# Kernel optimization log

Hardware: AMD Instinct MI355X
Metric: run time of the kernel (lower is better)

The kernel has to match this reference:

```python
import jax, jax.numpy as jnp
import numpy as np
import math

EPS = float(jnp.finfo(jnp.float32).eps)


def _mask_imag(z, n_ops):
    # Zero the imaginary part of (b,c) slices whose relative imaginary
    # magnitude is below the FFT roundoff threshold (vectorized version of
    # the original per-(i,j) Python loop).
    re, im = z.real, z.imag
    max_im = jnp.max(jnp.abs(im), axis=(-2, -1), keepdims=True)
    max_abs = jnp.max(jnp.abs(z), axis=(-2, -1), keepdims=True)
    mask = (max_im / max_abs) <= (n_ops * EPS)
    im = jnp.where(mask, jnp.zeros_like(im), im)
    return jax.lax.complex(re, im)


def otf2psf(otf, outsize):
    h, w = otf.shape[-2], otf.shape[-1]
    n_ops = h * w * (math.log2(h) + math.log2(w))
    psf = jnp.fft.ifft2(otf)
    psf = _mask_imag(psf, n_ops)
    psf = jnp.roll(psf, (outsize[0] // 2, outsize[1] // 2), axis=(-2, -1))
    return psf[..., : outsize[0], : outsize[1]]


def psf2otf(psf, shape):
    p0, p1 = psf.shape[-2], psf.shape[-1]
    n_ops = p0 * p1 * (math.log2(p0) + math.log2(p1))
    pad = [(0, 0)] * (psf.ndim - 2) + [(0, shape[0] - p0), (0, shape[1] - p1)]
    otf = jnp.pad(psf, pad)
    otf = jnp.roll(otf, (-(p0 // 2), -(p1 // 2)), axis=(-2, -1))
    otf = jnp.fft.fft2(otf)
    return _mask_imag(otf, n_ops)


def compute_ax(psf, latent_ft, image_size, psf_size_2d, gamma):
    xf = psf2otf(psf, image_size)          # [b, cp, H, W] complex
    y = jnp.real(otf2psf(latent_ft * xf, psf_size_2d))  # [b, c, p, p]
    return y + gamma * psf


def conjgrad(x, latent_ft, b_rhs, n_iter, image_size, psf_size_2d, gamma):
    r = b_rhs - compute_ax(x, latent_ft, image_size, psf_size_2d, gamma)
    p = r
    rsold = jnp.sum(r * r, axis=(-2, -1), keepdims=True)
    for _ in range(n_iter):  # small fixed iteration count
        Ap = compute_ax(p, latent_ft, image_size, psf_size_2d, gamma)
        alpha = rsold / jnp.sum(p * Ap, axis=(-2, -1), keepdims=True)
        x = x + alpha * p
        r = r - alpha * Ap
        rsnew = jnp.sum(r * r, axis=(-2, -1), keepdims=True)
        p = r + (rsnew / rsold) * p
        rsold = rsnew
    return x


def setup_inputs() -> dict:
    key = jax.random.key(0)
    k1, k2, k3, k4 = jax.random.split(key, 4)
    shape = (4, 3, 512, 512)
    return {
        "blurx": jax.random.normal(k1, shape, dtype=jnp.float32),
        "blury": jax.random.normal(k2, shape, dtype=jnp.float32),
        "latentx": jax.random.normal(k3, shape, dtype=jnp.float32),
        "latenty": jax.random.normal(k4, shape, dtype=jnp.float32),
        "psf_size": 31,
    }


def reference(blurx, blury, latentx, latenty, psf_size):
    n_iter = 10
    gamma = 1.0
    blur = jnp.sqrt(blurx ** 2 + blury ** 2)
    latent = jnp.sqrt(latentx ** 2 + latenty ** 2)
    b, c, h, w = blur.shape
    kernel = jnp.full((b, 1, psf_size, psf_size), 1.0 / float(psf_size ** 2), dtype=blur.dtype)
    blur_f = jnp.fft.fft2(blur)
    latent_f = jnp.fft.fft2(latent)
    bf = jnp.conj(latent_f) * blur_f
    latent_ft = jnp.conj(latent_f) * latent_f
    blur_otf = jnp.real(otf2psf(bf, (psf_size, psf_size)))  # [b, c, p, p]
    kernel = conjgrad(kernel, latent_ft, blur_otf, n_iter, (h, w), (psf_size, psf_size), gamma)
    # threshold small entries, clamp negatives, normalize
    kf = kernel.reshape(b, c, -1)
    max_var = jnp.max(kf, axis=2, keepdims=True)
    kf = jnp.where(kf < 0.05 * max_var, jnp.zeros_like(kf), kf)
    kernel = kf.reshape(b, c, psf_size, psf_size)
    kernel = jnp.where(kernel < 0, jnp.zeros_like(kernel), kernel)
    kernel = kernel / jnp.sum(kernel, axis=(-2, -1), keepdims=True)
    return kernel
```

## Files before the change

### kernel.cpp

```cpp
#include <hip/hip_runtime.h>
#include <math.h>

#define NIMG 12
#define NN 512
#define NPIX (NN * NN)

__device__ __forceinline__ int brev9(int p) {
  return (int)(__brev((unsigned)p) >> 23);
}

__device__ __forceinline__ void fft512_core(
    float vr[8], float vi[8], const int inv,
    const float* __restrict__ twr, const float* __restrict__ twi,
    const int lane)
{
#pragma unroll
  for (int s = 0; s < 3; ++s) {
    const int half = 1 << s;
#pragma unroll
    for (int e = 0; e < 8; ++e) {
      if ((e & half) == 0) {
        const int j = (e & (half - 1)) << (8 - s);
        const float wr = twr[j];
        const float wi = inv ? -twi[j] : twi[j];
        const float br = vr[e + half], bi = vi[e + half];
        const float tr = __fsub_rn(__fmul_rn(wr, br), __fmul_rn(wi, bi));
        const float ti = __fadd_rn(__fmul_rn(wr, bi), __fmul_rn(wi, br));
        vr[e + half] = __fsub_rn(vr[e], tr); vi[e + half] = __fsub_rn(vi[e], ti);
        vr[e] = __fadd_rn(vr[e], tr); vi[e] = __fadd_rn(vi[e], ti);
      }
    }
  }
#pragma unroll
  for (int s = 3; s <= 8; ++s) {
    const int xm = 1 << (s - 3);
    const bool low = (lane & xm) == 0;
#pragma unroll
    for (int e = 0; e < 8; ++e) {
      const float orr = __shfl_xor(vr[e], xm);
      const float oii = __shfl_xor(vi[e], xm);
      const int j = ((((lane & (xm - 1)) << 3) | e)) << (8 - s);
      const float wr = twr[j];
      const float wi = inv ? -twi[j] : twi[j];
      if (low) {
        const float tr = __fsub_rn(__fmul_rn(wr, orr), __fmul_rn(wi, oii));
        const float ti = __fadd_rn(__fmul_rn(wr, oii), __fmul_rn(wi, orr));
        vr[e] = __fadd_rn(vr[e], tr); vi[e] = __fadd_rn(vi[e], ti);
      } else {
        const float tr = __fsub_rn(__fmul_rn(wr, vr[e]), __fmul_rn(wi, vi[e]));
        const float ti = __fadd_rn(__fmul_rn(wr, vi[e]), __fmul_rn(wi, vr[e]));
        vr[e] = __fsub_rn(orr, tr); vi[e] = __fsub_rn(oii, ti);
      }
    }
  }
  if (inv) {
    const float sc = 1.0f / 512.0f;
#pragma unroll
    for (int e = 0; e < 8; ++e) {
      vr[e] = __fmul_rn(vr[e], sc); vi[e] = __fmul_rn(vi[e], sc);
    }
  }
}

__device__ __forceinline__ float np_pw_base(const float* a, int n)
{
  float r0 = a[0], r1 = a[1], r2 = a[2], r3 = a[3];
  float r4 = a[4], r5 = a[5], r6 = a[6], r7 = a[7];
  int i = 8;
  const int lim = n - (n & 7);
  for (; i < lim; i += 8) {
    r0 = __fadd_rn(r0, a[i + 0]); r1 = __fadd_rn(r1, a[i + 1]);
    r2 = __fadd_rn(r2, a[i + 2]); r3 = __fadd_rn(r3, a[i + 3]);
    r4 = __fadd_rn(r4, a[i + 4]); r5 = __fadd_rn(r5, a[i + 5]);
    r6 = __fadd_rn(r6, a[i + 6]); r7 = __fadd_rn(r7, a[i + 7]);
  }
  float res = __fadd_rn(
      __fadd_rn(__fadd_rn(r0, r1), __fadd_rn(r2, r3)),
      __fadd_rn(__fadd_rn(r4, r5), __fadd_rn(r6, r7)));
  for (; i < n; ++i) res = __fadd_rn(res, a[i]);
  return res;
}

__global__ __launch_bounds__(256) void twiddle_kernel(float2* __restrict__ twg)
{
  const int k = threadIdx.x;
  double s, c;
  sincos(-2.0 * M_PI * (double)k / 512.0, &s, &c);
  twg[k] = make_float2((float)c, (float)s);
}

__global__ __launch_bounds__(256) void loadmag_kernel(
    const float* __restrict__ bx, const float* __restrict__ by,
    const float* __restrict__ lx, const float* __restrict__ ly,
    float2* __restrict__ B2, float2* __restrict__ B1)
{
  const int i = blockIdx.x * 256 + threadIdx.x;
  {
    const float a = lx[i], b = ly[i];
    const float s = __fadd_rn(__fmul_rn(a, a), __fmul_rn(b, b));
    B2[i] = make_float2((float)sqrt((double)s), 0.f);
  }
  {
    const float a = bx[i], b = by[i];
    const float s = __fadd_rn(__fmul_rn(a, a), __fmul_rn(b, b));
    B1[i] = make_float2((float)sqrt((double)s), 0.f);
  }
}

__global__ __launch_bounds__(256) void rowfft_kernel(
    float2* __restrict__ A, float2* __restrict__ B,
    const float2* __restrict__ twg)
{
  __shared__ float twr[256], twi[256];
  { const float2 t = twg[threadIdx.x]; twr[threadIdx.x] = t.x; twi[threadIdx.x] = t.y; }
  __syncthreads();
  int wid = blockIdx.x * 4 + (threadIdx.x >> 6);
  const int lane = threadIdx.x & 63;
  float2* buf = A;
  if (wid >= NIMG * NN) { wid -= NIMG * NN; buf = B; }
  const int base = (wid >> 9) * NPIX + (wid & 511) * NN;
  float vr[8], vi[8];
#pragma unroll
  for (int e = 0; e < 8; ++e) {
    const float2 z = buf[base + brev9(lane * 8 + e)];
    vr[e] = z.x; vi[e] = z.y;
  }
  fft512_core(vr, vi, 0, twr, twi, lane);
#pragma unroll
  for (int e = 0; e < 8; ++e)
    buf[base + lane * 8 + e] = make_float2(vr[e], vi[e]);
}

__global__ __launch_bounds__(256) void colA_kernel(
    float2* __restrict__ B2, const float2* __restrict__ twg)
{
  __shared__ float twr[256], twi[256];
  __shared__ float2 ld[4][520];
  { const float2 t = twg[threadIdx.x]; twr[threadIdx.x] = t.x; twi[threadIdx.x] = t.y; }
  const int img = blockIdx.x >> 7;
  const int c0  = (blockIdx.x & 127) * 4;
  const int tid = threadIdx.x;
  float2* __restrict__ base = B2 + img * NPIX;
  for (int it = 0; it < 8; ++it) {
    const int idx = it * 256 + tid;
    ld[idx & 3][idx >> 2] = base[(idx >> 2) * NN + c0 + (idx & 3)];
  }
  __syncthreads();
  const int w = tid >> 6, lane = tid & 63;
  float vr[8], vi[8];
#pragma unroll
  for (int e = 0; e < 8; ++e) {
    const float2 z = ld[w][brev9(lane * 8 + e)];
    vr[e] = z.x; vi[e] = z.y;
  }
  fft512_core(vr, vi, 0, twr, twi, lane);
#pragma unroll
  for (int e = 0; e < 8; ++e) ld[w][lane * 8 + e] = make_float2(vr[e], vi[e]);
  __syncthreads();
  for (int it = 0; it < 8; ++it) {
    const int idx = it * 256 + tid;
    base[(idx >> 2) * NN + c0 + (idx & 3)] = ld[idx & 3][idx >> 2];
  }
}

__global__ __launch_bounds__(256) void colB_kernel(
    const float2* __restrict__ B1, float2* __restrict__ B3,
    const float2* __restrict__ twg)
{
  __shared__ float twr[256], twi[256];
  __shared__ float2 ld[4][520];
  { const float2 t = twg[threadIdx.x]; twr[threadIdx.x] = t.x; twi[threadIdx.x] = t.y; }
  const int img = blockIdx.x >> 7;
  const int c0  = (blockIdx.x & 127) * 4;
  const int tid = threadIdx.x;
  const float2* __restrict__ in = B1 + img * NPIX;
  for (int it = 0; it < 8; ++it) {
    const int idx = it * 256 + tid;
    ld[idx & 3][idx >> 2] = in[(idx >> 2) * NN + c0 + (idx & 3)];
  }
  __syncthreads();
  const int w = tid >> 6, lane = tid & 63;
  const int c = c0 + w;
  float vr[8], vi[8];
#pragma unroll
  for (int e = 0; e < 8; ++e) {
    const float2 z = ld[w][brev9(lane * 8 + e)];
    vr[e] = z.x; vi[e] = z.y;
  }
  fft512_core(vr, vi, 0, twr, twi, lane);
  float2* __restrict__ out = B3 + img * NPIX + c * NN + lane * 8;
#pragma unroll
  for (int e = 0; e < 8; ++e) out[e] = make_float2(vr[e], vi[e]);
}

__global__ __launch_bounds__(256) void fp_kernel(
    const float2* __restrict__ B2, float* __restrict__ FP)
{
  const int i = blockIdx.x * 256 + threadIdx.x;
  const float2 l = B2[i];
  FP[i] = __fadd_rn(__fmul_rn(l.x, l.x), __fmul_rn(l.y, l.y));
}

__global__ __launch_bounds__(256) void kb_kernel(
    const float2* __restrict__ R, float2* __restrict__ B3,
    unsigned* __restrict__ stats, const float2* __restrict__ twg)
{
  __shared__ float twr[256], twi[256];
  __shared__ float smi[4], sma[4];
  { const float2 t = twg[threadIdx.x]; twr[threadIdx.x] = t.x; twi[threadIdx.x] = t.y; }
  __syncthreads();
  const int img = blockIdx.x >> 7;
  const int c   = (blockIdx.x & 127) * 4 + (threadIdx.x >> 6);
  const int lane = threadIdx.x & 63;
  float vr[8], vi[8];
#pragma unroll
  for (int e = 0; e < 8; ++e) {
    const int q = brev9(lane * 8 + e);
    const int k = (q + 15) & 511;
    if (k < 31) {
      const float2 z = R[(img * 31 + k) * NN + c];
      vr[e] = z.x; vi[e] = z.y;
    } else { vr[e] = 0.f; vi[e] = 0.f; }
  }
  fft512_core(vr, vi, 0, twr, twi, lane);
  float mi = 0.f, ma = 0.f;
#pragma unroll
  for (int e = 0; e < 8; ++e) {
    mi = fmaxf(mi, fabsf(vi[e]));
    const float ab = (float)sqrt(
        (double)__fadd_rn(__fmul_rn(vr[e], vr[e]), __fmul_rn(vi[e], vi[e])));
    ma = fmaxf(ma, ab);
  }
#pragma unroll
  for (int off = 32; off; off >>= 1) {
    mi = fmaxf(mi, __shfl_xor(mi, off));
    ma = fmaxf(ma, __shfl_xor(ma, off));
  }
  if (lane == 0) { smi[threadIdx.x >> 6] = mi; sma[threadIdx.x >> 6] = ma; }
  float2* __restrict__ out = B3 + img * NPIX + c * NN + lane * 8;
#pragma unroll
  for (int e = 0; e < 8; ++e) out[e] = make_float2(vr[e], vi[e]);
  __syncthreads();
  if (threadIdx.x == 0) {
    mi = fmaxf(fmaxf(smi[0], smi[1]), fmaxf(smi[2], smi[3]));
    ma = fmaxf(fmaxf(sma[0], sma[1]), fmaxf(sma[2], sma[3]));
    atomicMax(&stats[img * 2 + 0], __float_as_uint(mi));
    atomicMax(&stats[img * 2 + 1], __float_as_uint(ma));
  }
}

__global__ __launch_bounds__(256) void kprod_kernel(
    const float2* __restrict__ B3, const float2* __restrict__ B2,
    const float* __restrict__ FP, float2* __restrict__ Y,
    const unsigned* __restrict__ stats, const float2* __restrict__ twg,
    int bmode)
{
  __shared__ float twr[256], twi[256];
  __shared__ float2 ldx[8][520];
  { const float2 t = twg[threadIdx.x]; twr[threadIdx.x] = t.x; twi[threadIdx.x] = t.y; }
  const int img = blockIdx.x >> 6;
  const int r0  = (blockIdx.x & 63) * 8;
  const int tid = threadIdx.x;
  const float2* __restrict__ X = B3 + img * NPIX;
  for (int it = 0; it < 16; ++it) {
    const int idx = it * 256 + tid;
    ldx[idx & 7][idx >> 3] = X[(idx >> 3) * NN + r0 + (idx & 7)];
  }
  bool fire = false;
  if (bmode == 0) {
    const float m1 = __uint_as_float(stats[img * 2 + 0]);
    const float m2 = __uint_as_float(stats[img * 2 + 1]);
    const double MTHR =
        961.0 * (log2(31.0) + log2(31.0)) * 1.1920928955078125e-7;
    fire = ((double)__fdiv_rn(m1, m2) <= MTHR);
  }
  __syncthreads();
  const int w = tid >> 6, lane = tid & 63;
  for (int rep = 0; rep < 2; ++rep) {
    const int r_l = w + 4 * rep;
    const int r = r0 + r_l;
    float vr[8], vi[8];
    if (bmode) {
      const float2* __restrict__ Lrow = B2 + img * NPIX + r * NN;
#pragma unroll
      for (int e = 0; e < 8; ++e) {
        const int q = brev9(lane * 8 + e);
        const float2 xb = ldx[r_l][q];
        const float2 l  = Lrow[q];
        vr[e] = __fadd_rn(__fmul_rn(l.x, xb.x), __fmul_rn(l.y, xb.y));
        vi[e] = __fsub_rn(__fmul_rn(l.x, xb.y), __fmul_rn(l.y, xb.x));
      }
    } else {
      const float* __restrict__ Frow = FP + img * NPIX + r * NN;
#pragma unroll
      for (int e = 0; e < 8; ++e) {
        const int q = brev9(lane * 8 + e);
        const float2 xb = ldx[r_l][q];
        const float fi = fire ? 0.f : xb.y;
        const float F  = Frow[q];
        vr[e] = __fmul_rn(F, xb.x);
        vi[e] = __fmul_rn(F, fi);
      }
    }
    fft512_core(vr, vi, 1, twr, twi, lane);
#pragma unroll
    for (int e = 0; e < 8; ++e) {
      const int c2 = lane * 8 + e;
      if (c2 >= 497 || c2 <= 15) {
        const int v = (c2 + 15) & 511;
        Y[(img * 31 + v) * NN + r] = make_float2(vr[e], vi[e]);
      }
    }
  }
}

__global__ __launch_bounds__(256) void kA_kernel(
    const float2* __restrict__ Y, float* __restrict__ yv,
    const float2* __restrict__ twg)
{
  __shared__ float twr[256], twi[256];
  { const float2 t = twg[threadIdx.x]; twr[threadIdx.x] = t.x; twi[threadIdx.x] = t.y; }
  __syncthreads();
  const int wid = blockIdx.x * 4 + (threadIdx.x >> 6);
  if (wid >= NIMG * 31) return;
  const int lane = threadIdx.x & 63;
  const int img = wid / 31, v = wid - img * 31;
  const float2* __restrict__ Yv = Y + (img * 31 + v) * NN;
  float vr[8], vi[8];
#pragma unroll
  for (int e = 0; e < 8; ++e) {
    const float2 z = Yv[brev9(lane * 8 + e)];
    vr[e] = z.x; vi[e] = z.y;
  }
  fft512_core(vr, vi, 1, twr, twi, lane);
#pragma unroll
  for (int e = 0; e < 8; ++e) {
    const int q2 = lane * 8 + e;
    const int u = (q2 + 15) & 511;
    if (u < 31) yv[img * 961 + u * 31 + v] = vr[e];
  }
}

__global__ __launch_bounds__(1024) void kC_kernel(
    const float* __restrict__ yv, float2* __restrict__ R,
    float* __restrict__ bvec, float* __restrict__ xv,
    float* __restrict__ rv, float* __restrict__ pv,
    float* __restrict__ rsoldg, unsigned* __restrict__ stats,
    const float2* __restrict__ twg, float* __restrict__ out,
    int mode, int fin)
{
  __shared__ float twr[256], twi[256];
  __shared__ float pl[961], prodl[961];
  __shared__ float pwl[8], redf[16];
  __shared__ float scal;
  const int tid = threadIdx.x;
  const int wave = tid >> 6, lane = tid & 63;
  const int img = blockIdx.x;
  if (tid < 256) { const float2 t = twg[tid]; twr[tid] = t.x; twi[tid] = t.y; }
  __syncthreads();

  const bool act = tid < 961;
  const int g = img * 961 + tid;

  auto pairwise = [&]() -> float {
    __syncthreads();
    if (tid < 8) pwl[tid] = np_pw_base(prodl + tid * 120, (tid == 7) ? 121 : 120);
    __syncthreads();
    if (tid == 0) {
      const float L = __fadd_rn(__fadd_rn(pwl[0], pwl[1]), __fadd_rn(pwl[2], pwl[3]));
      const float Rr = __fadd_rn(__fadd_rn(pwl[4], pwl[5]), __fadd_rn(pwl[6], pwl[7]));
      scal = __fadd_rn(L, Rr);
    }
    __syncthreads();
    const float s = scal;
    __syncthreads();
    return s;
  };

  if (mode == 2) {
    if (act) {
      bvec[g] = yv[g];
      xv[g] = (float)(1.0 / 961.0);
      pl[tid] = (float)(1.0 / 961.0);
    }
  } else if (mode == 0) {
    if (act) {
      const float Ap = __fadd_rn(yv[g], xv[g]);
      const float r0 = __fsub_rn(bvec[g], Ap);
      rv[g] = r0; pv[g] = r0; pl[tid] = r0;
      prodl[tid] = __fmul_rn(r0, r0);
    }
    const float s = pairwise();
    if (tid == 0) rsoldg[img] = s;
  } else {
    float p = 0.f, Ap = 0.f, nr = 0.f;
    if (act) {
      p = pv[g];
      Ap = __fadd_rn(yv[g], p);
      prodl[tid] = __fmul_rn(p, Ap);
    }
    const float pAp = pairwise();
    if (tid == 0) scal = rsoldg[img] / pAp;
    __syncthreads();
    const float alpha = scal;
    __syncthreads();
    if (act) {
      xv[g] = __fadd_rn(xv[g], __fmul_rn(alpha, p));
      nr = __fsub_rn(rv[g], __fmul_rn(alpha, Ap));
      rv[g] = nr;
      prodl[tid] = __fmul_rn(nr, nr);
    }
    const float rsnew = pairwise();
    if (tid == 0) { scal = rsnew / rsoldg[img]; rsoldg[img] = rsnew; }
    __syncthreads();
    const float beta = scal;
    __syncthreads();
    if (act) {
      const float pn = __fadd_rn(nr, __fmul_rn(beta, p));
      pv[g] = pn; pl[tid] = pn;
    }
  }
  if (tid == 0) { stats[img * 2 + 0] = 0u; stats[img * 2 + 1] = 0u; }
  __syncthreads();

  if (fin) {
    const float x = act ? xv[g] : -3.4e38f;
    float v = x;
#pragma unroll
    for (int off = 32; off; off >>= 1) v = fmaxf(v, __shfl_xor(v, off));
    if (lane == 0) redf[wave] = v;
    __syncthreads();
    if (tid == 0) {
      float s = redf[0];
      for (int w2 = 1; w2 < 16; ++w2) s = fmaxf(s, redf[w2]);
      scal = s;
    }
    __syncthreads();
    const float maxv = scal;
    const float thrf = __fmul_rn(0.05f, maxv);
    float vvv = act ? x : 0.f;
    if (vvv < thrf) vvv = 0.f;
    if (vvv < 0.f)  vvv = 0.f;
    if (act) prodl[tid] = vvv;
    const float ssum = pairwise();
    if (act) out[g] = vvv / ssum;
    return;
  }

  for (int rep = 0; rep < 2; ++rep) {
    const int k = wave + 16 * rep;
    if (k < 31) {
      float vr[8], vi[8];
#pragma unroll
      for (int e = 0; e < 8; ++e) {
        const int q = brev9(lane * 8 + e);
        const int l = (q + 15) & 511;
        vr[e] = (l < 31) ? pl[k * 31 + l] : 0.f;
        vi[e] = 0.f;
      }
      fft512_core(vr, vi, 0, twr, twi, lane);
      float2* __restrict__ Rk = R + (img * 31 + k) * NN + lane * 8;
#pragma unroll
      for (int e = 0; e < 8; ++e) Rk[e] = make_float2(vr[e], vi[e]);
    }
  }
}

extern "C" void kernel_launch(void* const* d_in, const int* in_sizes, int n_in,
                              void* d_out, int out_size, void* d_ws, size_t ws_size,
                              hipStream_t stream)
{
  const float* bx = (const float*)d_in[0];
  const float* by = (const float*)d_in[1];
  const float* lx = (const float*)d_in[2];
  const float* ly = (const float*)d_in[3];

  float* ws = (float*)d_ws;
  float2* B1 = (float2*)ws;
  float2* B2 = B1 + (size_t)NIMG * NPIX;
  float2* B3 = B2 + (size_t)NIMG * NPIX;
  float2* R  = B3 + (size_t)NIMG * NPIX;
  float2* Y  = R  + (size_t)NIMG * 31 * NN;
  float*  FP = (float*)(Y + (size_t)NIMG * 31 * NN);
  float*  vec = FP + (size_t)NIMG * NPIX;
  float*  bvec = vec;
  float*  xv   = bvec + NIMG * 961;
  float*  rv   = xv   + NIMG * 961;
  float*  pv   = rv   + NIMG * 961;
  float*  yv   = pv   + NIMG * 961;
  float*  rsold = yv  + NIMG * 961;
  unsigned* stats = (unsigned*)(rsold + NIMG);
  float2* twg = (float2*)(stats + 24);
  float* out = (float*)d_out;

  twiddle_kernel<<<1, 256, 0, stream>>>(twg);
  loadmag_kernel<<<NIMG * NPIX / 256, 256, 0, stream>>>(bx, by, lx, ly, B2, B1);
  rowfft_kernel<<<2 * NIMG * NN / 4, 256, 0, stream>>>(B2, B1, twg);
  colA_kernel<<<NIMG * 128, 256, 0, stream>>>(B2, twg);
  colB_kernel<<<NIMG * 128, 256, 0, stream>>>(B1, B3, twg);
  fp_kernel<<<NIMG * NPIX / 256, 256, 0, stream>>>(B2, FP);
  kprod_kernel<<<NIMG * 64, 256, 0, stream>>>(B3, B2, FP, Y, stats, twg, 1);
  kA_kernel<<<(NIMG * 31 + 3) / 4, 256, 0, stream>>>(Y, yv, twg);
  kC_kernel<<<NIMG, 1024, 0, stream>>>(yv, R, bvec, xv, rv, pv, rsold, stats,
                                       twg, out, 2, 0);

  for (int a = 0; a < 11; ++a) {
    kb_kernel<<<NIMG * 128, 256, 0, stream>>>(R, B3, stats, twg);
    kprod_kernel<<<NIMG * 64, 256, 0, stream>>>(B3, B2, FP, Y, stats, twg, 0);
    kA_kernel<<<(NIMG * 31 + 3) / 4, 256, 0, stream>>>(Y, yv, twg);
    const int mode = (a == 0) ? 0 : 1;
    const int fin  = (a == 10) ? 1 : 0;
    kC_kernel<<<NIMG, 1024, 0, stream>>>(yv, R, bvec, xv, rv, pv, rsold, stats,
                                         twg, out, mode, fin);
  }
}
```

Measured before the change: 1.458 ms.

## Exploit Hermitian symmetry to store and compute only half the column FFT spectrum

The column FFT kernels (colB, kb) now compute and store only columns 0..256 of the real-input spectrum, roughly halving their FFT work and memory writes. kprod rebuilds the other half on the fly from conjugate-symmetric entries, loading paired rows r and 512-r into a shared tile so each block handles 16 rows. This cuts global traffic and FFT work in the repeated CG loop. The cost is more complex indexing, a larger shared tile, fewer kprod blocks, and a dependence on the inputs to those FFTs being real.

```diff
diff --git a/kernel.cpp b/kernel.cpp
--- a/kernel.cpp
+++ b/kernel.cpp
@@ -4,6 +4,7 @@
 #define NIMG 12
 #define NN 512
 #define NPIX (NN * NN)
+#define XST (257 * 512)
 
 __device__ __forceinline__ int brev9(int p) {
   return (int)(__brev((unsigned)p) >> 23);
@@ -164,23 +165,25 @@
 }
 
 __global__ __launch_bounds__(256) void colB_kernel(
-    const float2* __restrict__ B1, float2* __restrict__ B3,
+    const float2* __restrict__ B1, float2* __restrict__ XH,
     const float2* __restrict__ twg)
 {
   __shared__ float twr[256], twi[256];
   __shared__ float2 ld[4][520];
   { const float2 t = twg[threadIdx.x]; twr[threadIdx.x] = t.x; twi[threadIdx.x] = t.y; }
-  const int img = blockIdx.x >> 7;
-  const int c0  = (blockIdx.x & 127) * 4;
+  const int img = blockIdx.x / 65;
+  const int c0  = (blockIdx.x % 65) * 4;
   const int tid = threadIdx.x;
   const float2* __restrict__ in = B1 + img * NPIX;
   for (int it = 0; it < 8; ++it) {
     const int idx = it * 256 + tid;
-    ld[idx & 3][idx >> 2] = in[(idx >> 2) * NN + c0 + (idx & 3)];
+    const int cc = c0 + (idx & 3);
+    ld[idx & 3][idx >> 2] = in[(idx >> 2) * NN + (cc < NN ? cc : NN - 1)];
   }
   __syncthreads();
   const int w = tid >> 6, lane = tid & 63;
   const int c = c0 + w;
+  if (c > 256) return;
   float vr[8], vi[8];
 #pragma unroll
   for (int e = 0; e < 8; ++e) {
@@ -188,7 +191,7 @@
     vr[e] = z.x; vi[e] = z.y;
   }
   fft512_core(vr, vi, 0, twr, twi, lane);
-  float2* __restrict__ out = B3 + img * NPIX + c * NN + lane * 8;
+  float2* __restrict__ out = XH + (size_t)img * XST + c * NN + lane * 8;
 #pragma unroll
   for (int e = 0; e < 8; ++e) out[e] = make_float2(vr[e], vi[e]);
 }
@@ -202,34 +205,39 @@
 }
 
 __global__ __launch_bounds__(256) void kb_kernel(
-    const float2* __restrict__ R, float2* __restrict__ B3,
+    const float2* __restrict__ R, float2* __restrict__ XH,
     unsigned* __restrict__ stats, const float2* __restrict__ twg)
 {
   __shared__ float twr[256], twi[256];
   __shared__ float smi[4], sma[4];
   { const float2 t = twg[threadIdx.x]; twr[threadIdx.x] = t.x; twi[threadIdx.x] = t.y; }
   __syncthreads();
-  const int img = blockIdx.x >> 7;
-  const int c   = (blockIdx.x & 127) * 4 + (threadIdx.x >> 6);
+  const int img = blockIdx.x / 65;
+  const int c   = (blockIdx.x % 65) * 4 + (threadIdx.x >> 6);
   const int lane = threadIdx.x & 63;
-  float vr[8], vi[8];
-#pragma unroll
-  for (int e = 0; e < 8; ++e) {
-    const int q = brev9(lane * 8 + e);
-    const int k = (q + 15) & 511;
-    if (k < 31) {
-      const float2 z = R[(img * 31 + k) * NN + c];
-      vr[e] = z.x; vi[e] = z.y;
-    } else { vr[e] = 0.f; vi[e] = 0.f; }
-  }
-  fft512_core(vr, vi, 0, twr, twi, lane);
   float mi = 0.f, ma = 0.f;
-#pragma unroll
-  for (int e = 0; e < 8; ++e) {
-    mi = fmaxf(mi, fabsf(vi[e]));
-    const float ab = (float)sqrt(
-        (double)__fadd_rn(__fmul_rn(vr[e], vr[e]), __fmul_rn(vi[e], vi[e])));
-    ma = fmaxf(ma, ab);
+  if (c <= 256) {
+    float vr[8], vi[8];
+#pragma unroll
+    for (int e = 0; e < 8; ++e) {
+      const int q = brev9(lane * 8 + e);
+      const int k = (q + 15) & 511;
+      if (k < 31) {
+        const float2 z = R[(img * 31 + k) * NN + c];
+        vr[e] = z.x; vi[e] = z.y;
+      } else { vr[e] = 0.f; vi[e] = 0.f; }
+    }
+    fft512_core(vr, vi, 0, twr, twi, lane);
+#pragma unroll
+    for (int e = 0; e < 8; ++e) {
+      mi = fmaxf(mi, fabsf(vi[e]));
+      const float ab = (float)sqrt(
+          (double)__fadd_rn(__fmul_rn(vr[e], vr[e]), __fmul_rn(vi[e], vi[e])));
+      ma = fmaxf(ma, ab);
+    }
+    float2* __restrict__ out = XH + (size_t)img * XST + c * NN + lane * 8;
+#pragma unroll
+    for (int e = 0; e < 8; ++e) out[e] = make_float2(vr[e], vi[e]);
   }
 #pragma unroll
   for (int off = 32; off; off >>= 1) {
@@ -237,9 +245,6 @@
     ma = fmaxf(ma, __shfl_xor(ma, off));
   }
   if (lane == 0) { smi[threadIdx.x >> 6] = mi; sma[threadIdx.x >> 6] = ma; }
-  float2* __restrict__ out = B3 + img * NPIX + c * NN + lane * 8;
-#pragma unroll
-  for (int e = 0; e < 8; ++e) out[e] = make_float2(vr[e], vi[e]);
   __syncthreads();
   if (threadIdx.x == 0) {
     mi = fmaxf(fmaxf(smi[0], smi[1]), fmaxf(smi[2], smi[3]));
@@ -250,21 +255,27 @@
 }
 
 __global__ __launch_bounds__(256) void kprod_kernel(
-    const float2* __restrict__ B3, const float2* __restrict__ B2,
+    const float2* __restrict__ XH, const float2* __restrict__ B2,
     const float* __restrict__ FP, float2* __restrict__ Y,
     const unsigned* __restrict__ stats, const float2* __restrict__ twg,
     int bmode)
 {
   __shared__ float twr[256], twi[256];
-  __shared__ float2 ldx[8][520];
+  __shared__ float2 T[17][257];
   { const float2 t = twg[threadIdx.x]; twr[threadIdx.x] = t.x; twi[threadIdx.x] = t.y; }
-  const int img = blockIdx.x >> 6;
-  const int r0  = (blockIdx.x & 63) * 8;
+  const int img = blockIdx.x >> 5;
+  const int g   = blockIdx.x & 31;
   const int tid = threadIdx.x;
-  const float2* __restrict__ X = B3 + img * NPIX;
-  for (int it = 0; it < 16; ++it) {
-    const int idx = it * 256 + tid;
-    ldx[idx & 7][idx >> 3] = X[(idx >> 3) * NN + r0 + (idx & 7)];
+  const float2* __restrict__ Xi = XH + (size_t)img * XST;
+  const int base1 = 8 * g;
+  const int base2 = (g == 0) ? 504 : (505 - 8 * g);
+  for (int idx = tid; idx < 257 * 16; idx += 256) {
+    const int c = idx >> 4, sub = idx & 15;
+    const int row = (sub < 8) ? (base1 + (sub & 7)) : (base2 + (sub & 7));
+    T[sub][c] = Xi[c * NN + row];
+  }
+  if (g == 0) {
+    for (int c = tid; c < 257; c += 256) T[16][c] = Xi[c * NN + 256];
   }
   bool fire = false;
   if (bmode == 0) {
@@ -276,17 +287,28 @@
   }
   __syncthreads();
   const int w = tid >> 6, lane = tid & 63;
-  for (int rep = 0; rep < 2; ++rep) {
-    const int r_l = w + 4 * rep;
-    const int r = r0 + r_l;
+  for (int t = 0; t < 4; ++t) {
+    const int oi = w + 4 * t;
+    int r, slot_r, slot_m;
+    if (g == 0) {
+      if (oi < 8)       { r = oi;       slot_r = oi;     slot_m = (oi == 0) ? 0 : (16 - oi); }
+      else if (oi < 15) { r = 497 + oi; slot_r = oi + 1; slot_m = 15 - oi; }
+      else              { r = 256;      slot_r = 16;     slot_m = 16; }
+    } else {
+      r = (oi < 8) ? (base1 + oi) : (base2 + (oi - 8));
+      slot_r = oi;
+      slot_m = 15 - oi;
+    }
     float vr[8], vi[8];
     if (bmode) {
       const float2* __restrict__ Lrow = B2 + img * NPIX + r * NN;
 #pragma unroll
       for (int e = 0; e < 8; ++e) {
         const int q = brev9(lane * 8 + e);
-        const float2 xb = ldx[r_l][q];
-        const float2 l  = Lrow[q];
+        float2 xb;
+        if (q <= 256) xb = T[slot_r][q];
+        else { const float2 tt = T[slot_m][512 - q]; xb = make_float2(tt.x, -tt.y); }
+        const float2 l = Lrow[q];
         vr[e] = __fadd_rn(__fmul_rn(l.x, xb.x), __fmul_rn(l.y, xb.y));
         vi[e] = __fsub_rn(__fmul_rn(l.x, xb.y), __fmul_rn(l.y, xb.x));
       }
@@ -295,7 +317,9 @@
 #pragma unroll
       for (int e = 0; e < 8; ++e) {
         const int q = brev9(lane * 8 + e);
-        const float2 xb = ldx[r_l][q];
+        float2 xb;
+        if (q <= 256) xb = T[slot_r][q];
+        else { const float2 tt = T[slot_m][512 - q]; xb = make_float2(tt.x, -tt.y); }
         const float fi = fire ? 0.f : xb.y;
         const float F  = Frow[q];
         vr[e] = __fmul_rn(F, xb.x);
@@ -478,8 +502,8 @@
   float* ws = (float*)d_ws;
   float2* B1 = (float2*)ws;
   float2* B2 = B1 + (size_t)NIMG * NPIX;
-  float2* B3 = B2 + (size_t)NIMG * NPIX;
-  float2* R  = B3 + (size_t)NIMG * NPIX;
+  float2* XH = B2 + (size_t)NIMG * NPIX;
+  float2* R  = XH + (size_t)NIMG * XST;
   float2* Y  = R  + (size_t)NIMG * 31 * NN;
   float*  FP = (float*)(Y + (size_t)NIMG * 31 * NN);
   float*  vec = FP + (size_t)NIMG * NPIX;
@@ -497,16 +521,16 @@
   loadmag_kernel<<<NIMG * NPIX / 256, 256, 0, stream>>>(bx, by, lx, ly, B2, B1);
   rowfft_kernel<<<2 * NIMG * NN / 4, 256, 0, stream>>>(B2, B1, twg);
   colA_kernel<<<NIMG * 128, 256, 0, stream>>>(B2, twg);
-  colB_kernel<<<NIMG * 128, 256, 0, stream>>>(B1, B3, twg);
+  colB_kernel<<<NIMG * 65, 256, 0, stream>>>(B1, XH, twg);
   fp_kernel<<<NIMG * NPIX / 256, 256, 0, stream>>>(B2, FP);
-  kprod_kernel<<<NIMG * 64, 256, 0, stream>>>(B3, B2, FP, Y, stats, twg, 1);
+  kprod_kernel<<<NIMG * 32, 256, 0, stream>>>(XH, B2, FP, Y, stats, twg, 1);
   kA_kernel<<<(NIMG * 31 + 3) / 4, 256, 0, stream>>>(Y, yv, twg);
   kC_kernel<<<NIMG, 1024, 0, stream>>>(yv, R, bvec, xv, rv, pv, rsold, stats,
                                        twg, out, 2, 0);
 
   for (int a = 0; a < 11; ++a) {
-    kb_kernel<<<NIMG * 128, 256, 0, stream>>>(R, B3, stats, twg);
-    kprod_kernel<<<NIMG * 64, 256, 0, stream>>>(B3, B2, FP, Y, stats, twg, 0);
+    kb_kernel<<<NIMG * 65, 256, 0, stream>>>(R, XH, stats, twg);
+    kprod_kernel<<<NIMG * 32, 256, 0, stream>>>(XH, B2, FP, Y, stats, twg, 0);
     kA_kernel<<<(NIMG * 31 + 3) / 4, 256, 0, stream>>>(Y, yv, twg);
     const int mode = (a == 0) ? 0 : 1;
     const int fin  = (a == 10) ? 1 : 0;
```

New measurement: 1.487 ms. No clear change (+2.0%).
